# Performance work log

Hardware: AMD Instinct MI355X
Metric: run time of the kernel (lower is better)

Reference implementation:

```python
import jax, jax.numpy as jnp
import numpy as np

N = 250000   # atoms
E = 500000   # directed bond edges
B = 10000    # molecules
IN = 39      # atom feature dim (in_channels)
H = 128      # hidden_channels
ED = 10      # edge_dim
NUM_TIMESTEPS = 2


def setup_inputs() -> dict:
    key = jax.random.key(0)
    ks = iter(jax.random.split(key, 40))
    p = lambda shape: jax.random.normal(next(ks), shape, dtype=jnp.float32) * 0.05
    inp = {}
    inp["x"] = jax.random.normal(next(ks), (N, IN), dtype=jnp.float32)
    inp["edge_attr"] = jax.random.normal(next(ks), (E, ED), dtype=jnp.float32)
    # lin1
    inp["W_lin1"] = p((H, IN)); inp["b_lin1"] = p((H,))
    # GATEConv
    inp["gate_W1"] = p((H, H + ED)); inp["gate_W2"] = p((H, H))
    inp["gate_att_l"] = p((H,)); inp["gate_att_r"] = p((H,)); inp["gate_bias"] = p((H,))
    # GRUCell after GATEConv
    inp["gru1_Wih"] = p((3 * H, H)); inp["gru1_Whh"] = p((3 * H, H))
    inp["gru1_bih"] = p((3 * H,)); inp["gru1_bhh"] = p((3 * H,))
    # atom GATConv (num_layers-1 == 1)
    inp["conv_W"] = p((H, H)); inp["conv_att_src"] = p((H,)); inp["conv_att_dst"] = p((H,)); inp["conv_bias"] = p((H,))
    inp["gru2_Wih"] = p((3 * H, H)); inp["gru2_Whh"] = p((3 * H, H))
    inp["gru2_bih"] = p((3 * H,)); inp["gru2_bhh"] = p((3 * H,))
    # mol GATConv (bipartite atoms -> molecules, shared lin)
    inp["mol_W"] = p((H, H)); inp["mol_att_src"] = p((H,)); inp["mol_att_dst"] = p((H,)); inp["mol_bias"] = p((H,))
    inp["grum_Wih"] = p((3 * H, H)); inp["grum_Whh"] = p((3 * H, H))
    inp["grum_bih"] = p((3 * H,)); inp["grum_bhh"] = p((3 * H,))
    # lin2 + head
    inp["W_lin2"] = p((H, H)); inp["b_lin2"] = p((H,))
    inp["W_head"] = p((1, H)); inp["b_head"] = p((1,))
    inp["edge_index"] = jax.random.randint(next(ks), (2, E), 0, N, dtype=jnp.int32)
    inp["batch"] = jnp.sort(jax.random.randint(next(ks), (N,), 0, B, dtype=jnp.int32))
    return inp


def _gru(xg, hg, Wih, Whh, bih, bhh):
    # torch.nn.GRUCell semantics
    gi = xg @ Wih.T + bih
    gh = hg @ Whh.T + bhh
    ir, iz, inn = jnp.split(gi, 3, axis=-1)
    hr, hz, hn = jnp.split(gh, 3, axis=-1)
    r = jax.nn.sigmoid(ir + hr)
    z = jax.nn.sigmoid(iz + hz)
    n = jnp.tanh(inn + r * hn)
    return (1.0 - z) * n + z * hg


def _seg_softmax(logits, seg, num):
    # PyG softmax over target-index segments (stable, +1e-16 denom)
    m = jax.ops.segment_max(logits, seg, num_segments=num)
    e = jnp.exp(logits - m[seg])
    s = jax.ops.segment_sum(e, seg, num_segments=num)
    return e / (s[seg] + 1e-16)


def reference(x, edge_attr, W_lin1, b_lin1, gate_W1, gate_W2, gate_att_l, gate_att_r, gate_bias,
              gru1_Wih, gru1_Whh, gru1_bih, gru1_bhh,
              conv_W, conv_att_src, conv_att_dst, conv_bias,
              gru2_Wih, gru2_Whh, gru2_bih, gru2_bhh,
              mol_W, mol_att_src, mol_att_dst, mol_bias,
              grum_Wih, grum_Whh, grum_bih, grum_bhh,
              W_lin2, b_lin2, W_head, b_head,
              edge_index, batch):
    lrelu = lambda v: jax.nn.leaky_relu(v, 0.01)
    src, dst = edge_index[0], edge_index[1]  # (j, i): messages flow j -> i
    # initial atom embedding
    x = lrelu(x @ W_lin1.T + b_lin1)
    # ---- GATEConv (edge-attr-aware attention, aggr='add') ----
    xj = x[src]                                                   # [E, H]
    he = lrelu(jnp.concatenate([xj, edge_attr], axis=-1) @ gate_W1.T)
    alpha = lrelu(he @ gate_att_l + x[dst] @ gate_att_r)          # [E]
    alpha = _seg_softmax(alpha, dst, N)
    h = jax.ops.segment_sum((xj @ gate_W2.T) * alpha[:, None], dst, num_segments=N) + gate_bias
    h = jax.nn.elu(h)
    x = jax.nn.relu(_gru(h, x, gru1_Wih, gru1_Whh, gru1_bih, gru1_bhh))
    # ---- atom GATConv (heads=1, neg_slope=0.01, no self loops) ----
    xl = x @ conv_W.T
    a = lrelu((xl * conv_att_src).sum(-1)[src] + (xl * conv_att_dst).sum(-1)[dst])
    a = _seg_softmax(a, dst, N)
    h = jax.ops.segment_sum(xl[src] * a[:, None], dst, num_segments=N) + conv_bias
    h = jax.nn.relu(h)
    x = jax.nn.relu(_gru(h, x, gru2_Wih, gru2_Whh, gru2_bih, gru2_bhh))
    # ---- attentive graph readout: bipartite GAT atoms -> molecules ----
    out = jax.nn.relu(jax.ops.segment_sum(x, batch, num_segments=B))  # [B, H]
    for _ in range(NUM_TIMESTEPS):
        xs = x @ mol_W.T                                          # src transform [N, H]
        od = out @ mol_W.T                                        # dst transform [B, H]
        a = lrelu((xs * mol_att_src).sum(-1) + ((od * mol_att_dst).sum(-1))[batch])
        a = _seg_softmax(a, batch, B)
        h = jax.ops.segment_sum(xs * a[:, None], batch, num_segments=B) + mol_bias
        h = jax.nn.elu(h)
        out = jax.nn.relu(_gru(h, out, grum_Wih, grum_Whh, grum_bih, grum_bhh))
    out = out @ W_lin2.T + b_lin2
    out = out @ W_head.T + b_head                                 # [B, 1]
    return out.squeeze(-1)                                        # [B]
```

## Files before the change

### kernel.cpp

```cpp
#include <hip/hip_runtime.h>
#include <hip/hip_bf16.h>
#include <type_traits>

typedef __hip_bfloat16 bf16;

constexpr int N_  = 250000;
constexpr int E_  = 500000;
constexpr int B_  = 10000;
constexpr int H_  = 128;

typedef short s8v __attribute__((ext_vector_type(8)));
typedef float f4v __attribute__((ext_vector_type(4)));

__device__ __forceinline__ float b2f(bf16 v){ return __bfloat162float(v); }
__device__ __forceinline__ bf16  f2b(float v){ return __float2bfloat16(v); }
__device__ __forceinline__ float lrelu_f(float v){ return v > 0.f ? v : 0.01f*v; }
__device__ __forceinline__ float sigmoid_f(float x){ return __builtin_amdgcn_rcpf(1.f+__expf(-x)); }
__device__ __forceinline__ float tanh_f(float x){ return 1.f - 2.f*__builtin_amdgcn_rcpf(__expf(2.f*x)+1.f); }
__device__ __forceinline__ float elu_f(float v){ return v > 0.f ? v : __expf(v)-1.f; }
__device__ __forceinline__ unsigned f2b_bits(float f){
  bf16 h=__float2bfloat16(f); unsigned short s; __builtin_memcpy(&s,&h,2); return (unsigned)s;
}
__device__ __forceinline__ void unp8(uint4 v, float* o){
  o[0]=__uint_as_float(v.x<<16); o[1]=__uint_as_float(v.x&0xffff0000u);
  o[2]=__uint_as_float(v.y<<16); o[3]=__uint_as_float(v.y&0xffff0000u);
  o[4]=__uint_as_float(v.z<<16); o[5]=__uint_as_float(v.z&0xffff0000u);
  o[6]=__uint_as_float(v.w<<16); o[7]=__uint_as_float(v.w&0xffff0000u);
}

struct W2B { const float* s; bf16* d; int rows, ld, ow, cw; };
struct W2B9 { W2B seg[9]; };
__global__ void w2ball_k(W2B9 p){
  W2B g=p.seg[blockIdx.y];
  int i=blockIdx.x*256+threadIdx.x;
  if (i>=g.rows*g.ow) return;
  int r=i/g.ow, k=i-r*g.ow;
  g.d[i] = f2b(k<g.cw ? g.s[(size_t)r*g.ld+k] : 0.f);
}

__global__ __launch_bounds__(256) void lin1_mfma_k(const float* __restrict__ X0, const bf16* __restrict__ Wb,
                            const float* __restrict__ bias, const float* __restrict__ dvec,
                            bf16* __restrict__ Y, float* __restrict__ dout, int M){
  __shared__ __align__(16) bf16 sx[64][72];
  __shared__ float sdot[4][64];
  int wv=threadIdx.x>>6, lane=threadIdx.x&63;
  int n=lane&15, q=lane>>4;
  int c0=wv*32;
  s8v wB[2][2];
  #pragma unroll
  for (int ct=0;ct<2;ct++)
    #pragma unroll
    for (int kk=0;kk<2;kk++)
      wB[ct][kk]=*(const s8v*)(Wb+(size_t)(c0+ct*16+n)*64+kk*32+q*8);
  float bb[2];
  #pragma unroll
  for (int ct=0;ct<2;ct++) bb[ct]=bias[c0+ct*16+n];
  float va[2]={dvec[c0+n], dvec[c0+16+n]};
  for (int i=threadIdx.x;i<64*25;i+=256){ int r=i/25,k=39+(i-(i/25)*25); sx[r][k]=f2b(0.f); }
  for (long r0=(long)blockIdx.x*64; r0<M; r0+=(long)gridDim.x*64){
    __syncthreads();
    for (int f=threadIdx.x; f<64*39; f+=256){
      int r=f/39, k=f-(f/39)*39; long row=r0+r;
      sx[r][k]= f2b(row<M ? X0[row*39+k] : 0.f);
    }
    __syncthreads();
    s8v a[4][2];
    #pragma unroll
    for (int rt=0;rt<4;rt++)
      #pragma unroll
      for (int kk=0;kk<2;kk++)
        a[rt][kk]=*(const s8v*)&sx[rt*16+n][kk*32+q*8];
    f4v acc[4][2];
    #pragma unroll
    for (int rt=0;rt<4;rt++)
      #pragma unroll
      for (int ct=0;ct<2;ct++) acc[rt][ct]=(f4v){0.f,0.f,0.f,0.f};
    #pragma unroll
    for (int kk=0;kk<2;kk++)
      #pragma unroll
      for (int rt=0;rt<4;rt++)
        #pragma unroll
        for (int ct=0;ct<2;ct++)
          acc[rt][ct]=__builtin_amdgcn_mfma_f32_16x16x32_bf16(a[rt][kk],wB[ct][kk],acc[rt][ct],0,0,0);
    #pragma unroll
    for (int rt=0;rt<4;rt++){
      #pragma unroll
      for (int rg=0;rg<4;rg++){
        float y0=lrelu_f(acc[rt][0][rg]+bb[0]);
        float y1=lrelu_f(acc[rt][1][rg]+bb[1]);
        long row=r0+rt*16+q*4+rg;
        if (row<M){
          Y[row*128+c0+n]   =f2b(y0);
          Y[row*128+c0+16+n]=f2b(y1);
        }
        float pa=y0*va[0]+y1*va[1];
        #pragma unroll
        for (int o=1;o<16;o<<=1) pa+=__shfl_xor(pa,o);
        if (n==0) sdot[wv][rt*16+q*4+rg]=pa;
      }
    }
    __syncthreads();
    if (threadIdx.x<64){
      long row=r0+threadIdx.x;
      if (row<M) dout[row]=sdot[0][threadIdx.x]+sdot[1][threadIdx.x]+sdot[2][threadIdx.x]+sdot[3][threadIdx.x];
    }
  }
}

template<int ACT,int NDOT>
__global__ __launch_bounds__(256) void lin_mfma_k(const bf16* __restrict__ X, const bf16* __restrict__ Wb,
                            const float* __restrict__ bias, bf16* __restrict__ Y,
                            const float* __restrict__ v1, const float* __restrict__ v2,
                            float* __restrict__ d1, float* __restrict__ d2, int M){
  __shared__ float sdot[2][4][64];
  int wv=threadIdx.x>>6, lane=threadIdx.x&63;
  int n=lane&15, q=lane>>4;
  int c0=wv*32;
  s8v wB[2][4];
  #pragma unroll
  for (int ct=0;ct<2;ct++)
    #pragma unroll
    for (int kk=0;kk<4;kk++)
      wB[ct][kk]=*(const s8v*)(Wb+(size_t)(c0+ct*16+n)*128+kk*32+q*8);
  float bb[2];
  #pragma unroll
  for (int ct=0;ct<2;ct++) bb[ct]=bias? bias[c0+ct*16+n]:0.f;
  float va[2][2];
  if constexpr (NDOT>=1){ va[0][0]=v1[c0+n]; va[0][1]=v1[c0+16+n]; }
  if constexpr (NDOT>=2){ va[1][0]=v2[c0+n]; va[1][1]=v2[c0+16+n]; }
  for (long r0=(long)blockIdx.x*64; r0<M; r0+=(long)gridDim.x*64){
    s8v a[4][4];
    #pragma unroll
    for (int rt=0;rt<4;rt++){
      long row=r0+rt*16+n; if (row>=M) row=M-1;
      #pragma unroll
      for (int kk=0;kk<4;kk++) a[rt][kk]=*(const s8v*)(X+row*128+kk*32+q*8);
    }
    f4v acc[4][2];
    #pragma unroll
    for (int rt=0;rt<4;rt++)
      #pragma unroll
      for (int ct=0;ct<2;ct++) acc[rt][ct]=(f4v){0.f,0.f,0.f,0.f};
    #pragma unroll
    for (int kk=0;kk<4;kk++)
      #pragma unroll
      for (int rt=0;rt<4;rt++)
        #pragma unroll
        for (int ct=0;ct<2;ct++)
          acc[rt][ct]=__builtin_amdgcn_mfma_f32_16x16x32_bf16(a[rt][kk],wB[ct][kk],acc[rt][ct],0,0,0);
    #pragma unroll
    for (int rt=0;rt<4;rt++){
      #pragma unroll
      for (int rg=0;rg<4;rg++){
        float y0=acc[rt][0][rg]+bb[0];
        float y1=acc[rt][1][rg]+bb[1];
        if (ACT==2){ y0=elu_f(y0); y1=elu_f(y1); }
        long row=r0+rt*16+q*4+rg;
        if (row<M){
          Y[row*128+c0+n]   =f2b(y0);
          Y[row*128+c0+16+n]=f2b(y1);
        }
        if constexpr (NDOT>=1){
          float pa=y0*va[0][0]+y1*va[0][1];
          float pb=0.f;
          if constexpr (NDOT>=2) pb=y0*va[1][0]+y1*va[1][1];
          #pragma unroll
          for (int o=1;o<16;o<<=1){
            pa+=__shfl_xor(pa,o);
            if constexpr (NDOT>=2) pb+=__shfl_xor(pb,o);
          }
          if (n==0){
            sdot[0][wv][rt*16+q*4+rg]=pa;
            if constexpr (NDOT>=2) sdot[1][wv][rt*16+q*4+rg]=pb;
          }
        }
      }
    }
    if constexpr (NDOT>=1){
      __syncthreads();
      if (threadIdx.x<64){
        long row=r0+threadIdx.x;
        if (row<M){
          d1[row]=sdot[0][0][threadIdx.x]+sdot[0][1][threadIdx.x]+sdot[0][2][threadIdx.x]+sdot[0][3][threadIdx.x];
          if constexpr (NDOT>=2)
            d2[row]=sdot[1][0][threadIdx.x]+sdot[1][1][threadIdx.x]+sdot[1][2][threadIdx.x]+sdot[1][3][threadIdx.x];
        }
      }
      __syncthreads();
    }
  }
}

__global__ __launch_bounds__(512,1) void gru_mfma_k(const bf16* __restrict__ A, const bf16* __restrict__ X,
                            const bf16* __restrict__ Wih, const bf16* __restrict__ Whh,
                            const float* __restrict__ bih, const float* __restrict__ bhh,
                            bf16* __restrict__ dest, int M){
  __shared__ __align__(16) bf16 sA[2][32][136];
  __shared__ __align__(16) bf16 sX[2][32][136];
  int wv=threadIdx.x>>6, lane=threadIdx.x&63;
  int n=lane&15, q=lane>>4;
  int c0=wv*16;
  s8v wI[3][4], wH[3][4];
  #pragma unroll
  for (int g=0;g<3;g++)
    #pragma unroll
    for (int kk=0;kk<4;kk++){
      size_t off=((size_t)(g*128+c0+n))*128+kk*32+q*8;
      wI[g][kk]=*(const s8v*)(Wih+off);
      wH[g][kk]=*(const s8v*)(Whh+off);
    }
  int col=c0+n;
  float br =bih[col]+bhh[col];
  float bz =bih[128+col]+bhh[128+col];
  float bni=bih[256+col], bnh=bhh[256+col];

  int srow=wv*4+q;
  int schunk=n;
  long step=(long)gridDim.x*32;
  long r0=(long)blockIdx.x*32;
  int buf=0;
  {
    long rowg=r0+srow; if (rowg>=M) rowg=M-1;
    uint4 va=*(const uint4*)(A+rowg*128+schunk*8);
    uint4 vx=*(const uint4*)(X+rowg*128+schunk*8);
    *(uint4*)&sA[0][srow][schunk*8]=va;
    *(uint4*)&sX[0][srow][schunk*8]=vx;
  }
  __syncthreads();
  for (; r0<M; r0+=step){
    long rn=r0+step;
    uint4 va, vx; bool pre = rn<M;
    if (pre){
      long rowg=rn+srow; if (rowg>=M) rowg=M-1;
      va=*(const uint4*)(A+rowg*128+schunk*8);
      vx=*(const uint4*)(X+rowg*128+schunk*8);
    }
    f4v acc[6][2];
    #pragma unroll
    for (int g=0;g<6;g++)
      #pragma unroll
      for (int rt=0;rt<2;rt++) acc[g][rt]=(f4v){0.f,0.f,0.f,0.f};
    #pragma unroll
    for (int kk=0;kk<4;kk++){
      s8v aA[2], aX[2];
      #pragma unroll
      for (int rt=0;rt<2;rt++){
        aA[rt]=*(const s8v*)&sA[buf][rt*16+n][(kk*4+q)*8];
        aX[rt]=*(const s8v*)&sX[buf][rt*16+n][(kk*4+q)*8];
      }
      #pragma unroll
      for (int g=0;g<3;g++)
        #pragma unroll
        for (int rt=0;rt<2;rt++){
          acc[g  ][rt]=__builtin_amdgcn_mfma_f32_16x16x32_bf16(aA[rt],wI[g][kk],acc[g  ][rt],0,0,0);
          acc[3+g][rt]=__builtin_amdgcn_mfma_f32_16x16x32_bf16(aX[rt],wH[g][kk],acc[3+g][rt],0,0,0);
        }
    }
    float xv[2][4];
    #pragma unroll
    for (int rt=0;rt<2;rt++)
      #pragma unroll
      for (int rg=0;rg<4;rg++)
        xv[rt][rg]=b2f(sX[buf][rt*16+q*4+rg][col]);
    #pragma unroll
    for (int rt=0;rt<2;rt++){
      #pragma unroll
      for (int rg=0;rg<4;rg++){
        long row=r0+rt*16+q*4+rg;
        if (row<M){
          float rgate=sigmoid_f(acc[0][rt][rg]+acc[3][rt][rg]+br);
          float zgate=sigmoid_f(acc[1][rt][rg]+acc[4][rt][rg]+bz);
          float nn=tanh_f(acc[2][rt][rg]+bni + rgate*(acc[5][rt][rg]+bnh));
          float o=(1.f-zgate)*nn + zgate*xv[rt][rg];
          dest[row*128+col]=f2b(fmaxf(o,0.f));
        }
      }
    }
    if (pre){
      *(uint4*)&sA[buf^1][srow][schunk*8]=va;
      *(uint4*)&sX[buf^1][srow][schunk*8]=vx;
    }
    __syncthreads();
    buf^=1;
  }
}

__global__ __launch_bounds__(256) void gru_scalar_k(const float* __restrict__ A, const float* __restrict__ X,
                            const float* __restrict__ Wih, const float* __restrict__ Whh,
                            const float* __restrict__ bih, const float* __restrict__ bhh,
                            float* __restrict__ dest, int M){
  __shared__ unsigned sW[6][32*66];
  __shared__ float sA[8][132], sX[8][132];
  __shared__ float sbi[3][32], sbh[3][32];
  int c0 = blockIdx.y*32;
  for (int i=threadIdx.x; i<6*32*64; i+=256){
    int m=i>>11, r=i&2047, c=r>>6, k2=r&63;
    const float* base = (m<3)? Wih : Whh;
    int g = (m<3)? m : m-3;
    const float* wp = base + ((size_t)(g*128 + c0 + c))*128 + 2*k2;
    sW[m][c*66 + k2] = f2b_bits(wp[0]) | (f2b_bits(wp[1])<<16);
  }
  if (threadIdx.x < 96){
    int g=threadIdx.x>>5, c=threadIdx.x&31;
    sbi[g][c]=bih[g*128+c0+c]; sbh[g][c]=bhh[g*128+c0+c];
  }
  __syncthreads();
  int sub=threadIdx.x>>5, c=threadIdx.x&31;
  for (long r0=(long)blockIdx.x*8; r0<M; r0+=(long)gridDim.x*8){
    __syncthreads();
    for (int i=threadIdx.x;i<8*16;i+=256){
      int rr=i>>4, q=i&15; long row=r0+rr;
      if (row<M){
        *(float4*)&sA[rr][q*8]   = *(const float4*)(A+row*128+q*8);
        *(float4*)&sA[rr][q*8+4] = *(const float4*)(A+row*128+q*8+4);
        *(float4*)&sX[rr][q*8]   = *(const float4*)(X+row*128+q*8);
        *(float4*)&sX[rr][q*8+4] = *(const float4*)(X+row*128+q*8+4);
      } else {
        float4 z=make_float4(0,0,0,0);
        *(float4*)&sA[rr][q*8]=z; *(float4*)&sA[rr][q*8+4]=z;
        *(float4*)&sX[rr][q*8]=z; *(float4*)&sX[rr][q*8+4]=z;
      }
    }
    __syncthreads();
    long row=r0+sub;
    if (row<M){
      const unsigned* wri=&sW[0][c*66]; const unsigned* wzi=&sW[1][c*66]; const unsigned* wni=&sW[2][c*66];
      const unsigned* wrh=&sW[3][c*66]; const unsigned* wzh=&sW[4][c*66]; const unsigned* wnh=&sW[5][c*66];
      const float2* xa=(const float2*)sA[sub]; const float2* xb=(const float2*)sX[sub];
      float ari=0,azi=0,ani=0,arh=0,azh=0,anh=0;
      #pragma unroll 8
      for (int k2=0;k2<64;k2++){
        float2 av=xa[k2], bv=xb[k2];
        unsigned u;
        u=wri[k2]; ari += av.x*__uint_as_float(u<<16) + av.y*__uint_as_float(u&0xffff0000u);
        u=wzi[k2]; azi += av.x*__uint_as_float(u<<16) + av.y*__uint_as_float(u&0xffff0000u);
        u=wni[k2]; ani += av.x*__uint_as_float(u<<16) + av.y*__uint_as_float(u&0xffff0000u);
        u=wrh[k2]; arh += bv.x*__uint_as_float(u<<16) + bv.y*__uint_as_float(u&0xffff0000u);
        u=wzh[k2]; azh += bv.x*__uint_as_float(u<<16) + bv.y*__uint_as_float(u&0xffff0000u);
        u=wnh[k2]; anh += bv.x*__uint_as_float(u<<16) + bv.y*__uint_as_float(u&0xffff0000u);
      }
      float rg = sigmoid_f(ari+arh+sbi[0][c]+sbh[0][c]);
      float zg = sigmoid_f(azi+azh+sbi[1][c]+sbh[1][c]);
      float nn = tanh_f(ani+sbi[2][c] + rg*(anh+sbh[2][c]));
      float xv = sX[sub][c0+c];
      float o  = (1.f-zg)*nn + zg*xv;
      dest[row*128+c0+c] = fmaxf(o,0.f);
    }
  }
}

__global__ __launch_bounds__(256) void gate_edge_logits_k(const bf16* __restrict__ u, const float* __restrict__ ea,
                                   const float* __restrict__ gW1, const float* __restrict__ att_l,
                                   const float* __restrict__ ddst, const int* __restrict__ src,
                                   const int* __restrict__ dst, const int* __restrict__ epos,
                                   float* __restrict__ elog, int E){
  int wv=threadIdx.x>>6, lane=threadIdx.x&63;
  int t=lane&31;
  float w[10][4];
  #pragma unroll
  for (int k=0;k<10;k++)
    #pragma unroll
    for (int j=0;j<4;j++)
      w[k][j]=gW1[(size_t)(t*4+j)*138 + 128 + k];
  float al[4];
  #pragma unroll
  for (int j=0;j<4;j++) al[j]=att_l[t*4+j];

  long stride=(long)gridDim.x*8;
  long e=(long)blockIdx.x*8 + wv*2 + (lane>>5);
  if (e>=E) return;
  int sj=src[e];
  uint2 uv=*(const uint2*)(u+(size_t)sj*128+t*4);
  const float2* er=(const float2*)(ea+(size_t)e*10);
  float2 c0=er[0],c1=er[1],c2=er[2],c3=er[3],c4=er[4];
  float dv=ddst[dst[e]];
  int ep=epos[e];
  while (true){
    long en=e+stride; bool has=en<E;
    uint2 uvn=make_uint2(0,0);
    float2 d0={0,0},d1={0,0},d2={0,0},d3={0,0},d4={0,0};
    float dvn=0.f; int epn=0;
    if (has){
      int sjn=src[en];
      uvn=*(const uint2*)(u+(size_t)sjn*128+t*4);
      const float2* ern=(const float2*)(ea+(size_t)en*10);
      d0=ern[0];d1=ern[1];d2=ern[2];d3=ern[3];d4=ern[4];
      dvn=ddst[dst[en]];
      epn=epos[en];
    }
    float uf[4];
    uf[0]=__uint_as_float(uv.x<<16); uf[1]=__uint_as_float(uv.x&0xffff0000u);
    uf[2]=__uint_as_float(uv.y<<16); uf[3]=__uint_as_float(uv.y&0xffff0000u);
    float acc=0.f;
    #pragma unroll
    for (int j=0;j<4;j++){
      float v=uf[j];
      v+=c0.x*w[0][j]; v+=c0.y*w[1][j];
      v+=c1.x*w[2][j]; v+=c1.y*w[3][j];
      v+=c2.x*w[4][j]; v+=c2.y*w[5][j];
      v+=c3.x*w[6][j]; v+=c3.y*w[7][j];
      v+=c4.x*w[8][j]; v+=c4.y*w[9][j];
      acc+=lrelu_f(v)*al[j];
    }
    #pragma unroll
    for (int o=16;o;o>>=1) acc+=__shfl_xor(acc,o);
    if (t==0) elog[ep]=lrelu_f(acc+dv);
    if (!has) break;
    e=en; uv=uvn; c0=d0;c1=d1;c2=d2;c3=d3;c4=d4; dv=dvn; ep=epn;
  }
}

template<int ACT>
__global__ void node_gather_k(const float* __restrict__ elog, const int* __restrict__ srcp,
                              const int* __restrict__ ptr, const bf16* __restrict__ V,
                              const float* __restrict__ bias, bf16* __restrict__ S, int M){
  int wv=threadIdx.x>>6, lane=threadIdx.x&63;
  int g=lane>>3, t=lane&7;
  int node=blockIdx.x*32 + wv*8 + g;
  if (node>=M) return;
  int p0=ptr[node], p1=ptr[node+1];
  float m=-INFINITY;
  for (int p=p0+t;p<p1;p+=8) m=fmaxf(m,elog[p]);
  #pragma unroll
  for (int o=4;o;o>>=1) m=fmaxf(m,__shfl_xor(m,o));
  float ssum=0.f;
  float acc[16]={0,0,0,0,0,0,0,0,0,0,0,0,0,0,0,0};
  if (p0<p1){
    float lg=elog[p0];
    const uint4* vp=(const uint4*)(V+(size_t)srcp[p0]*128+t*16);
    uint4 va=vp[0], vb=vp[1];
    for (int p=p0+1;p<p1;p++){
      float lgn=elog[p];
      const uint4* vpn=(const uint4*)(V+(size_t)srcp[p]*128+t*16);
      uint4 van=vpn[0], vbn=vpn[1];
      float e=__expf(lg-m); ssum+=e;
      float xf[8]; unp8(va,xf);
      #pragma unroll
      for (int j=0;j<8;j++) acc[j]+=e*xf[j];
      unp8(vb,xf);
      #pragma unroll
      for (int j=0;j<8;j++) acc[8+j]+=e*xf[j];
      lg=lgn; va=van; vb=vbn;
    }
    float e=__expf(lg-m); ssum+=e;
    float xf[8]; unp8(va,xf);
    #pragma unroll
    for (int j=0;j<8;j++) acc[j]+=e*xf[j];
    unp8(vb,xf);
    #pragma unroll
    for (int j=0;j<8;j++) acc[8+j]+=e*xf[j];
  }
  float inv=1.f/(ssum+1e-16f);
  #pragma unroll
  for (int j=0;j<16;j++) acc[j]*=inv;
  if (ACT==1){
    #pragma unroll
    for (int j=0;j<16;j++) acc[j]=fmaxf(acc[j]+bias[t*16+j],0.f);
  }
  uint4 o1,o2;
  o1.x=f2b_bits(acc[0])|(f2b_bits(acc[1])<<16);
  o1.y=f2b_bits(acc[2])|(f2b_bits(acc[3])<<16);
  o1.z=f2b_bits(acc[4])|(f2b_bits(acc[5])<<16);
  o1.w=f2b_bits(acc[6])|(f2b_bits(acc[7])<<16);
  o2.x=f2b_bits(acc[8])|(f2b_bits(acc[9])<<16);
  o2.y=f2b_bits(acc[10])|(f2b_bits(acc[11])<<16);
  o2.z=f2b_bits(acc[12])|(f2b_bits(acc[13])<<16);
  o2.w=f2b_bits(acc[14])|(f2b_bits(acc[15])<<16);
  *(uint4*)(S+(size_t)node*128+t*16)=o1;
  *(uint4*)(S+(size_t)node*128+t*16+8)=o2;
}

__global__ __launch_bounds__(256) void conv_gather_k(const float* __restrict__ dsrc, const float* __restrict__ ddst,
    const int* __restrict__ ptr, const int* __restrict__ srcp,
    const bf16* __restrict__ V, const float* __restrict__ bias, bf16* __restrict__ S, int M){
  int wv=threadIdx.x>>6, lane=threadIdx.x&63;
  int g=lane>>3, t=lane&7;
  int node=blockIdx.x*32 + wv*8 + g;
  if (node>=M) return;
  int p0=ptr[node], p1=ptr[node+1];
  float dvn=ddst[node];
  float m=-INFINITY, s=0.f;
  float acc[16]={0,0,0,0,0,0,0,0,0,0,0,0,0,0,0,0};
  if (p0<p1){
    int sj=srcp[p0];
    float ls=dsrc[sj];
    const uint4* vp=(const uint4*)(V+(size_t)sj*128+t*16);
    uint4 va=vp[0], vb=vp[1];
    for (int p=p0+1;p<p1;p++){
      int sjn=srcp[p];
      float lsn=dsrc[sjn];
      const uint4* vpn=(const uint4*)(V+(size_t)sjn*128+t*16);
      uint4 van=vpn[0], vbn=vpn[1];
      float l=lrelu_f(ls+dvn);
      float mn=fmaxf(m,l), sc=__expf(m-mn), ee=__expf(l-mn);
      float xf[8]; unp8(va,xf);
      s=s*sc+ee;
      #pragma unroll
      for (int j=0;j<8;j++) acc[j]=acc[j]*sc+ee*xf[j];
      unp8(vb,xf);
      #pragma unroll
      for (int j=0;j<8;j++) acc[8+j]=acc[8+j]*sc+ee*xf[j];
      m=mn; ls=lsn; va=van; vb=vbn;
    }
    float l=lrelu_f(ls+dvn);
    float mn=fmaxf(m,l), sc=__expf(m-mn), ee=__expf(l-mn);
    float xf[8]; unp8(va,xf);
    s=s*sc+ee;
    #pragma unroll
    for (int j=0;j<8;j++) acc[j]=acc[j]*sc+ee*xf[j];
    unp8(vb,xf);
    #pragma unroll
    for (int j=0;j<8;j++) acc[8+j]=acc[8+j]*sc+ee*xf[j];
  }
  float inv=1.f/(s+1e-16f);
  float r[16];
  #pragma unroll
  for (int j=0;j<16;j++) r[j]=fmaxf(acc[j]*inv+bias[t*16+j],0.f);
  uint4 o1,o2;
  o1.x=f2b_bits(r[0])|(f2b_bits(r[1])<<16);
  o1.y=f2b_bits(r[2])|(f2b_bits(r[3])<<16);
  o1.z=f2b_bits(r[4])|(f2b_bits(r[5])<<16);
  o1.w=f2b_bits(r[6])|(f2b_bits(r[7])<<16);
  o2.x=f2b_bits(r[8])|(f2b_bits(r[9])<<16);
  o2.y=f2b_bits(r[10])|(f2b_bits(r[11])<<16);
  o2.z=f2b_bits(r[12])|(f2b_bits(r[13])<<16);
  o2.w=f2b_bits(r[14])|(f2b_bits(r[15])<<16);
  *(uint4*)(S+(size_t)node*128+t*16)=o1;
  *(uint4*)(S+(size_t)node*128+t*16+8)=o2;
}

__global__ void mol_ptr_k(const int* __restrict__ batch, int* __restrict__ mptr, int n, int Bn){
  int b=blockIdx.x*256+threadIdx.x; if (b>Bn) return;
  if (b==Bn){ mptr[Bn]=n; return; }
  int lo=0, hi=n;
  while (lo<hi){ int mid=(lo+hi)>>1; if (batch[mid]<b) lo=mid+1; else hi=mid; }
  mptr[b]=lo;
}

__global__ void mol_sum_k(const bf16* __restrict__ x, const int* __restrict__ mptr,
                          float* __restrict__ out, int Bn){
  int wv=threadIdx.x>>6, lane=threadIdx.x&63;
  int b=blockIdx.x*4+wv; if (b>=Bn) return;
  int p0=mptr[b], p1=mptr[b+1];
  float a0=0.f,a1=0.f;
  for (int i=p0;i<p1;i++){ a0+=b2f(x[(size_t)i*128+lane]); a1+=b2f(x[(size_t)i*128+64+lane]); }
  out[(size_t)b*128+lane]=fmaxf(a0,0.f); out[(size_t)b*128+64+lane]=fmaxf(a1,0.f);
}

__global__ void fold_att_k(const float* __restrict__ W, const float* __restrict__ att,
                           float* __restrict__ wdd){
  int k=threadIdx.x; float a=0.f;
  for (int c=0;c<128;c++) a+=att[c]*W[(size_t)c*128+k];
  wdd[k]=a;
}

__global__ __launch_bounds__(256) void mol_fused_k(const float* __restrict__ dsrc, const int* __restrict__ mptr,
    const bf16* __restrict__ xs, const float* __restrict__ wdd, const float* __restrict__ outc,
    const float* __restrict__ bias, float* __restrict__ hb, int Bn){
  int wv=threadIdx.x>>6, lane=threadIdx.x&63;
  long b=(long)blockIdx.x*4+wv; if (b>=Bn) return;
  int p0=mptr[b], p1=mptr[b+1];
  float dd=outc[(size_t)b*128+lane]*wdd[lane]+outc[(size_t)b*128+64+lane]*wdd[64+lane];
  #pragma unroll
  for (int o=32;o;o>>=1) dd+=__shfl_xor(dd,o);
  float m=-INFINITY, s=0.f, a0=0.f, a1=0.f;
  for (int i=p0;i<p1;i++){
    float a=lrelu_f(dsrc[i]+dd);
    float x0=b2f(xs[(size_t)i*128+lane]), x1=b2f(xs[(size_t)i*128+64+lane]);
    float mn=fmaxf(m,a), sc=__expf(m-mn), ee=__expf(a-mn);
    s=s*sc+ee; a0=a0*sc+ee*x0; a1=a1*sc+ee*x1; m=mn;
  }
  float inv=1.f/(s+1e-16f);
  hb[(size_t)b*128+lane]=elu_f(a0*inv+bias[lane]);
  hb[(size_t)b*128+64+lane]=elu_f(a1*inv+bias[64+lane]);
}

__global__ void fold_head_k(const float* __restrict__ W2, const float* __restrict__ b2,
                            const float* __restrict__ Wh, const float* __restrict__ bh,
                            float* __restrict__ v){
  __shared__ float sred[128];
  int k=threadIdx.x;
  float a=0.f;
  for (int c=0;c<128;c++) a+=Wh[c]*W2[(size_t)c*128+k];
  v[k]=a;
  sred[k]=b2[k]*Wh[k]; __syncthreads();
  for (int o=64;o;o>>=1){ if (k<o) sred[k]+=sred[k+o]; __syncthreads(); }
  if (k==0) v[128]=sred[0]+bh[0];
}

__global__ void head_dot_k(const float* __restrict__ out, const float* __restrict__ v,
                           float* __restrict__ y, int M){
  __shared__ float sv[129];
  if (threadIdx.x<129) sv[threadIdx.x]=v[threadIdx.x];
  __syncthreads();
  int wv=threadIdx.x>>6, lane=threadIdx.x&63;
  long row=(long)blockIdx.x*4+wv;
  if (row>=M) return;
  float a=out[row*128+lane]*sv[lane]+out[row*128+64+lane]*sv[64+lane];
  #pragma unroll
  for (int o=32;o;o>>=1) a+=__shfl_xor(a,o);
  if (!lane) y[row]=a+sv[128];
}

__global__ void zero_i32_k(int* p, int n){ int i=blockIdx.x*256+threadIdx.x; if (i<n) p[i]=0; }
__global__ void hist_k(const int* __restrict__ dst, int* __restrict__ deg, int n){
  int e=blockIdx.x*256+threadIdx.x; if (e<n) atomicAdd(&deg[dst[e]],1);
}
__global__ void scan1_k(const int* __restrict__ deg, int* __restrict__ ptr,
                        int* __restrict__ part, int n){
  __shared__ int sd[256];
  int base=blockIdx.x*1024, tid=threadIdx.x;
  int v[4]; int ssum=0;
  #pragma unroll
  for (int j=0;j<4;j++){ int idx=base+tid*4+j; v[j]= idx<n? deg[idx]:0; ssum+=v[j]; }
  sd[tid]=ssum; __syncthreads();
  for (int o=1;o<256;o<<=1){ int t = tid>=o? sd[tid-o]:0; __syncthreads(); sd[tid]+=t; __syncthreads(); }
  int excl=sd[tid]-ssum;
  #pragma unroll
  for (int j=0;j<4;j++){ int idx=base+tid*4+j; if (idx<n) ptr[idx]=excl; excl+=v[j]; }
  if (tid==255) part[blockIdx.x]=sd[255];
}
__global__ void scan2_k(int* part, int nb){
  __shared__ int sd[512];
  int tid=threadIdx.x;
  int v= tid<nb? part[tid]:0; sd[tid]=v; __syncthreads();
  for (int o=1;o<512;o<<=1){ int t = tid>=o? sd[tid-o]:0; __syncthreads(); sd[tid]+=t; __syncthreads(); }
  if (tid<nb) part[tid]=sd[tid]-v;
}
__global__ void scan3_k(int* __restrict__ ptr, const int* __restrict__ part,
                        int* __restrict__ wofs, int n, int total){
  int i=blockIdx.x*256+threadIdx.x;
  if (i<n){ int val=ptr[i]+part[i>>10]; ptr[i]=val; wofs[i]=val; }
  if (i==0) ptr[n]=total;
}
__global__ void fill_csr_k(const int* __restrict__ dst, const int* __restrict__ src,
                           int* __restrict__ wofs, int* __restrict__ srcp,
                           int* __restrict__ epos, int n){
  int e=blockIdx.x*256+threadIdx.x;
  if (e<n){ int p=atomicAdd(&wofs[dst[e]],1); srcp[p]=src[e]; epos[e]=p; }
}

extern "C" void kernel_launch(void* const* d_in, const int* in_sizes, int n_in,
                              void* d_out, int out_size, void* d_ws, size_t ws_size,
                              hipStream_t stream){
  (void)in_sizes; (void)n_in; (void)out_size; (void)ws_size;
  const float* x0        =(const float*)d_in[0];
  const float* edge_attr =(const float*)d_in[1];
  const float* W_lin1    =(const float*)d_in[2];
  const float* b_lin1    =(const float*)d_in[3];
  const float* gate_W1   =(const float*)d_in[4];
  const float* gate_W2   =(const float*)d_in[5];
  const float* gate_att_l=(const float*)d_in[6];
  const float* gate_att_r=(const float*)d_in[7];
  const float* gate_bias =(const float*)d_in[8];
  const float* g1_Wih=(const float*)d_in[9];  const float* g1_Whh=(const float*)d_in[10];
  const float* g1_bih=(const float*)d_in[11]; const float* g1_bhh=(const float*)d_in[12];
  const float* conv_W=(const float*)d_in[13];
  const float* conv_att_src=(const float*)d_in[14];
  const float* conv_att_dst=(const float*)d_in[15];
  const float* conv_bias   =(const float*)d_in[16];
  const float* g2_Wih=(const float*)d_in[17]; const float* g2_Whh=(const float*)d_in[18];
  const float* g2_bih=(const float*)d_in[19]; const float* g2_bhh=(const float*)d_in[20];
  const float* mol_W=(const float*)d_in[21];
  const float* mol_att_src=(const float*)d_in[22];
  const float* mol_att_dst=(const float*)d_in[23];
  const float* mol_bias   =(const float*)d_in[24];
  const float* gm_Wih=(const float*)d_in[25]; const float* gm_Whh=(const float*)d_in[26];
  const float* gm_bih=(const float*)d_in[27]; const float* gm_bhh=(const float*)d_in[28];
  const float* W_lin2=(const float*)d_in[29]; const float* b_lin2=(const float*)d_in[30];
  const float* W_head=(const float*)d_in[31]; const float* b_head=(const float*)d_in[32];
  const int* ei   =(const int*)d_in[33];
  const int* batch=(const int*)d_in[34];
  const int* src=ei; const int* dst=ei+E_;
  float* y=(float*)d_out;

  const size_t NH=(size_t)N_*H_, BH=(size_t)B_*H_;
  bf16* b0  =(bf16*)d_ws;
  bf16* b1  =b0+NH;
  bf16* b2v =b1+NH;
  float* outA=(float*)(b2v+NH);
  float* outB=outA+BH;
  float* hb  =outB+BH;
  float* elog=hb+BH;
  float* dsrc=elog+E_;
  float* ddst=dsrc+N_;
  float* alog=ddst+N_;
  float* wdd =alog+N_;
  float* dd  =wdd+128;
  int* deg =(int*)(dd+B_);
  int* ptr =deg+N_;
  int* wofs=ptr+N_+1;
  int* part=wofs+N_;
  int* mptr=part+512;
  int* srcp=mptr+B_+1;
  int* epos=srcp+E_;
  uintptr_t wbase=((uintptr_t)(epos+E_)+255)&~(uintptr_t)255;
  bf16* wb_gw1 =(bf16*)wbase;
  bf16* wb_gw2 =wb_gw1 +128*128;
  bf16* wb_conv=wb_gw2 +128*128;
  bf16* wb_mol =wb_conv+128*128;
  bf16* wb_g1i =wb_mol +128*128;
  bf16* wb_g1h =wb_g1i +384*128;
  bf16* wb_g2i =wb_g1h +384*128;
  bf16* wb_g2h =wb_g2i +384*128;
  bf16* wb_l1  =wb_g2h +384*128;

  W2B9 wp;
  wp.seg[0]={gate_W1,wb_gw1,128,138,128,128};
  wp.seg[1]={gate_W2,wb_gw2,128,128,128,128};
  wp.seg[2]={conv_W ,wb_conv,128,128,128,128};
  wp.seg[3]={mol_W  ,wb_mol ,128,128,128,128};
  wp.seg[4]={g1_Wih,wb_g1i,384,128,128,128};
  wp.seg[5]={g1_Whh,wb_g1h,384,128,128,128};
  wp.seg[6]={g2_Wih,wb_g2i,384,128,128,128};
  wp.seg[7]={g2_Whh,wb_g2h,384,128,128,128};
  wp.seg[8]={W_lin1,wb_l1 ,128, 39, 64, 39};
  w2ball_k<<<dim3(192,9),256,0,stream>>>(wp);

  zero_i32_k<<<(N_+255)/256,256,0,stream>>>(deg,N_);
  hist_k<<<(E_+255)/256,256,0,stream>>>(dst,deg,E_);
  int nb=(N_+1023)/1024;
  scan1_k<<<nb,256,0,stream>>>(deg,ptr,part,N_);
  scan2_k<<<1,512,0,stream>>>(part,nb);
  scan3_k<<<(N_+255)/256,256,0,stream>>>(ptr,part,wofs,N_,E_);
  fill_csr_k<<<(E_+255)/256,256,0,stream>>>(dst,src,wofs,srcp,epos,E_);
  mol_ptr_k<<<(B_+1+255)/256,256,0,stream>>>(batch,mptr,N_,B_);

  lin1_mfma_k<<<1024,256,0,stream>>>(x0,wb_l1,b_lin1,gate_att_r,b0,ddst,N_);

  const int GL=768, GN8=(N_+31)/32;
  lin_mfma_k<0,0><<<GL,256,0,stream>>>(b0,wb_gw1,nullptr,b1,nullptr,nullptr,nullptr,nullptr,N_);
  gate_edge_logits_k<<<8192,256,0,stream>>>(b1,edge_attr,gate_W1,gate_att_l,ddst,src,dst,epos,elog,E_);
  node_gather_k<0><<<GN8,256,0,stream>>>(elog,srcp,ptr,b0,nullptr,b2v,N_);
  lin_mfma_k<2,0><<<GL,256,0,stream>>>(b2v,wb_gw2,gate_bias,b1,nullptr,nullptr,nullptr,nullptr,N_);
  gru_mfma_k<<<1024,512,0,stream>>>(b1,b0,wb_g1i,wb_g1h,g1_bih,g1_bhh,b2v,N_);
  lin_mfma_k<0,2><<<GL,256,0,stream>>>(b2v,wb_conv,nullptr,b0,conv_att_src,conv_att_dst,dsrc,ddst,N_);
  conv_gather_k<<<GN8,256,0,stream>>>(dsrc,ddst,ptr,srcp,b0,conv_bias,b1,N_);
  gru_mfma_k<<<1024,512,0,stream>>>(b1,b2v,wb_g2i,wb_g2h,g2_bih,g2_bhh,b0,N_);
  mol_sum_k<<<(B_+3)/4,256,0,stream>>>(b0,mptr,outA,B_);
  lin_mfma_k<0,1><<<GL,256,0,stream>>>(b0,wb_mol,nullptr,b1,mol_att_src,nullptr,dsrc,nullptr,N_);
  fold_att_k<<<1,128,0,stream>>>(mol_W,mol_att_dst,wdd);
  float* out_cur=outA; float* out_nxt=outB;
  dim3 gm(157,4);
  for (int ts=0; ts<2; ts++){
    mol_fused_k<<<(B_+3)/4,256,0,stream>>>(dsrc,mptr,b1,wdd,out_cur,mol_bias,hb,B_);
    gru_scalar_k<<<gm,256,0,stream>>>(hb,out_cur,gm_Wih,gm_Whh,gm_bih,gm_bhh,out_nxt,B_);
    float* tmp=out_cur; out_cur=out_nxt; out_nxt=tmp;
  }
  fold_head_k<<<1,128,0,stream>>>(W_lin2,b_lin2,W_head,b_head,elog);
  head_dot_k<<<(B_+3)/4,256,0,stream>>>(out_cur,elog,y,B_);
}
```

Measured before the change: 1.068 ms.

## Reassociate GAT linear transforms after aggregation and fuse into GRU kernels

Attention logits are now computed from folded vectors (W^T att) applied to the pre-transform features, so the full N×128 projection before each gather is no longer needed. Aggregation runs on the raw features, and the 128×128 linear, bias and activation are applied afterwards inside the GRU MFMA kernel, or in a small per-molecule kernel for the readout. This removes three full-size lin_mfma passes and their writes to global memory. In exchange it adds separate row-dot kernels that read the node features again, extra LDS and MFMA work plus a sync in the GRU kernel, and different bf16 rounding points.

```diff
diff --git a/kernel.cpp b/kernel.cpp
--- a/kernel.cpp
+++ b/kernel.cpp
@@ -14,6 +14,8 @@
 
 __device__ __forceinline__ float b2f(bf16 v){ return __bfloat162float(v); }
 __device__ __forceinline__ bf16  f2b(float v){ return __float2bfloat16(v); }
+__device__ __forceinline__ float to_float(float v){ return v; }
+__device__ __forceinline__ float to_float(bf16 v){ return __bfloat162float(v); }
 __device__ __forceinline__ float lrelu_f(float v){ return v > 0.f ? v : 0.01f*v; }
 __device__ __forceinline__ float sigmoid_f(float x){ return __builtin_amdgcn_rcpf(1.f+__expf(-x)); }
 __device__ __forceinline__ float tanh_f(float x){ return 1.f - 2.f*__builtin_amdgcn_rcpf(__expf(2.f*x)+1.f); }
@@ -36,6 +38,20 @@
   if (i>=g.rows*g.ow) return;
   int r=i/g.ow, k=i-r*g.ow;
   g.d[i] = f2b(k<g.cw ? g.s[(size_t)r*g.ld+k] : 0.f);
+}
+
+__global__ void fold4_k(const float* __restrict__ Wc, const float* __restrict__ cas,
+                        const float* __restrict__ cad, const float* __restrict__ Wm,
+                        const float* __restrict__ mas, const float* __restrict__ mad,
+                        float* __restrict__ w1c, float* __restrict__ w2c,
+                        float* __restrict__ wms, float* __restrict__ wdd){
+  int k=threadIdx.x; int which=blockIdx.x;
+  const float* W  = (which<2)? Wc : Wm;
+  const float* at = (which==0)? cas : (which==1)? cad : (which==2)? mas : mad;
+  float* out = (which==0)? w1c : (which==1)? w2c : (which==2)? wms : wdd;
+  float a=0.f;
+  for (int c=0;c<128;c++) a+=at[c]*W[(size_t)c*128+k];
+  out[k]=a;
 }
 
 __global__ __launch_bounds__(256) void lin1_mfma_k(const float* __restrict__ X0, const bf16* __restrict__ Wb,
@@ -107,12 +123,9 @@
   }
 }
 
-template<int ACT,int NDOT>
+template<int ACT>
 __global__ __launch_bounds__(256) void lin_mfma_k(const bf16* __restrict__ X, const bf16* __restrict__ Wb,
-                            const float* __restrict__ bias, bf16* __restrict__ Y,
-                            const float* __restrict__ v1, const float* __restrict__ v2,
-                            float* __restrict__ d1, float* __restrict__ d2, int M){
-  __shared__ float sdot[2][4][64];
+                            const float* __restrict__ bias, bf16* __restrict__ Y, int M){
   int wv=threadIdx.x>>6, lane=threadIdx.x&63;
   int n=lane&15, q=lane>>4;
   int c0=wv*32;
@@ -125,9 +138,6 @@
   float bb[2];
   #pragma unroll
   for (int ct=0;ct<2;ct++) bb[ct]=bias? bias[c0+ct*16+n]:0.f;
-  float va[2][2];
-  if constexpr (NDOT>=1){ va[0][0]=v1[c0+n]; va[0][1]=v1[c0+16+n]; }
-  if constexpr (NDOT>=2){ va[1][0]=v2[c0+n]; va[1][1]=v2[c0+16+n]; }
   for (long r0=(long)blockIdx.x*64; r0<M; r0+=(long)gridDim.x*64){
     s8v a[4][4];
     #pragma unroll
@@ -149,58 +159,69 @@
         for (int ct=0;ct<2;ct++)
           acc[rt][ct]=__builtin_amdgcn_mfma_f32_16x16x32_bf16(a[rt][kk],wB[ct][kk],acc[rt][ct],0,0,0);
     #pragma unroll
-    for (int rt=0;rt<4;rt++){
-      #pragma unroll
-      for (int rg=0;rg<4;rg++){
-        float y0=acc[rt][0][rg]+bb[0];
-        float y1=acc[rt][1][rg]+bb[1];
-        if (ACT==2){ y0=elu_f(y0); y1=elu_f(y1); }
-        long row=r0+rt*16+q*4+rg;
-        if (row<M){
-          Y[row*128+c0+n]   =f2b(y0);
-          Y[row*128+c0+16+n]=f2b(y1);
-        }
-        if constexpr (NDOT>=1){
-          float pa=y0*va[0][0]+y1*va[0][1];
-          float pb=0.f;
-          if constexpr (NDOT>=2) pb=y0*va[1][0]+y1*va[1][1];
-          #pragma unroll
-          for (int o=1;o<16;o<<=1){
-            pa+=__shfl_xor(pa,o);
-            if constexpr (NDOT>=2) pb+=__shfl_xor(pb,o);
-          }
-          if (n==0){
-            sdot[0][wv][rt*16+q*4+rg]=pa;
-            if constexpr (NDOT>=2) sdot[1][wv][rt*16+q*4+rg]=pb;
+    for (int ct=0;ct<2;ct++){
+      int col=c0+ct*16+n;
+      #pragma unroll
+      for (int rt=0;rt<4;rt++){
+        #pragma unroll
+        for (int rg=0;rg<4;rg++){
+          long row=r0+rt*16+q*4+rg;
+          if (row<M){
+            float v=acc[rt][ct][rg]+bb[ct];
+            if (ACT==2) v=elu_f(v);
+            Y[row*128+col]=f2b(v);
           }
         }
       }
     }
-    if constexpr (NDOT>=1){
-      __syncthreads();
-      if (threadIdx.x<64){
-        long row=r0+threadIdx.x;
-        if (row<M){
-          d1[row]=sdot[0][0][threadIdx.x]+sdot[0][1][threadIdx.x]+sdot[0][2][threadIdx.x]+sdot[0][3][threadIdx.x];
-          if constexpr (NDOT>=2)
-            d2[row]=sdot[1][0][threadIdx.x]+sdot[1][1][threadIdx.x]+sdot[1][2][threadIdx.x]+sdot[1][3][threadIdx.x];
-        }
-      }
-      __syncthreads();
-    }
-  }
-}
-
-__global__ __launch_bounds__(512,1) void gru_mfma_k(const bf16* __restrict__ A, const bf16* __restrict__ X,
+  }
+}
+
+template<typename TY>
+__global__ void rowdot_k(const TY* __restrict__ Y, const float* __restrict__ v,
+                         float* __restrict__ d, int M){
+  __shared__ float sv[128];
+  if (threadIdx.x<128) sv[threadIdx.x]=v[threadIdx.x];
+  __syncthreads();
+  int wv=threadIdx.x>>6, lane=threadIdx.x&63;
+  long row=(long)blockIdx.x*4+wv;
+  if (row>=M) return;
+  float a=to_float(Y[row*128+lane])*sv[lane]+to_float(Y[row*128+64+lane])*sv[64+lane];
+  #pragma unroll
+  for (int o=32;o;o>>=1) a+=__shfl_xor(a,o);
+  if (!lane) d[row]=a;
+}
+
+__global__ void rowdot2_k(const bf16* __restrict__ Y, const float* __restrict__ v1,
+                          const float* __restrict__ v2, float* __restrict__ d1,
+                          float* __restrict__ d2, int M){
+  __shared__ float sv1[128], sv2[128];
+  if (threadIdx.x<128){ sv1[threadIdx.x]=v1[threadIdx.x]; sv2[threadIdx.x]=v2[threadIdx.x]; }
+  __syncthreads();
+  int wv=threadIdx.x>>6, lane=threadIdx.x&63;
+  long row=(long)blockIdx.x*4+wv;
+  if (row>=M) return;
+  float x0=b2f(Y[row*128+lane]), x1=b2f(Y[row*128+64+lane]);
+  float a=x0*sv1[lane]+x1*sv1[64+lane];
+  float b=x0*sv2[lane]+x1*sv2[64+lane];
+  #pragma unroll
+  for (int o=32;o;o>>=1){ a+=__shfl_xor(a,o); b+=__shfl_xor(b,o); }
+  if (!lane){ d1[row]=a; d2[row]=b; }
+}
+
+template<int ACT>
+__global__ __launch_bounds__(512,1) void gru_gw2_mfma_k(const bf16* __restrict__ S, const bf16* __restrict__ X,
+                            const bf16* __restrict__ Wg, const float* __restrict__ gbias,
                             const bf16* __restrict__ Wih, const bf16* __restrict__ Whh,
                             const float* __restrict__ bih, const float* __restrict__ bhh,
                             bf16* __restrict__ dest, int M){
-  __shared__ __align__(16) bf16 sA[2][32][136];
+  __shared__ __align__(16) bf16 sS[2][32][136];
   __shared__ __align__(16) bf16 sX[2][32][136];
+  __shared__ __align__(16) bf16 sA[32][136];
   int wv=threadIdx.x>>6, lane=threadIdx.x&63;
   int n=lane&15, q=lane>>4;
   int c0=wv*16;
-  s8v wI[3][4], wH[3][4];
+  s8v wI[3][4], wH[3][4], wG[4];
   #pragma unroll
   for (int g=0;g<3;g++)
     #pragma unroll
@@ -209,7 +230,11 @@
       wI[g][kk]=*(const s8v*)(Wih+off);
       wH[g][kk]=*(const s8v*)(Whh+off);
     }
+  #pragma unroll
+  for (int kk=0;kk<4;kk++)
+    wG[kk]=*(const s8v*)(Wg+(size_t)(c0+n)*128+kk*32+q*8);
   int col=c0+n;
+  float bA =gbias[col];
   float br =bih[col]+bhh[col];
   float bz =bih[128+col]+bhh[128+col];
   float bni=bih[256+col], bnh=bhh[256+col];
@@ -221,20 +246,39 @@
   int buf=0;
   {
     long rowg=r0+srow; if (rowg>=M) rowg=M-1;
-    uint4 va=*(const uint4*)(A+rowg*128+schunk*8);
+    uint4 vs=*(const uint4*)(S+rowg*128+schunk*8);
     uint4 vx=*(const uint4*)(X+rowg*128+schunk*8);
-    *(uint4*)&sA[0][srow][schunk*8]=va;
+    *(uint4*)&sS[0][srow][schunk*8]=vs;
     *(uint4*)&sX[0][srow][schunk*8]=vx;
   }
   __syncthreads();
   for (; r0<M; r0+=step){
     long rn=r0+step;
-    uint4 va, vx; bool pre = rn<M;
+    uint4 vs, vx; bool pre = rn<M;
     if (pre){
       long rowg=rn+srow; if (rowg>=M) rowg=M-1;
-      va=*(const uint4*)(A+rowg*128+schunk*8);
+      vs=*(const uint4*)(S+rowg*128+schunk*8);
       vx=*(const uint4*)(X+rowg*128+schunk*8);
     }
+    f4v accA[2];
+    accA[0]=(f4v){0.f,0.f,0.f,0.f}; accA[1]=(f4v){0.f,0.f,0.f,0.f};
+    #pragma unroll
+    for (int kk=0;kk<4;kk++){
+      #pragma unroll
+      for (int rt=0;rt<2;rt++){
+        s8v aS=*(const s8v*)&sS[buf][rt*16+n][(kk*4+q)*8];
+        accA[rt]=__builtin_amdgcn_mfma_f32_16x16x32_bf16(aS,wG[kk],accA[rt],0,0,0);
+      }
+    }
+    #pragma unroll
+    for (int rt=0;rt<2;rt++)
+      #pragma unroll
+      for (int rg=0;rg<4;rg++){
+        float av=accA[rt][rg]+bA;
+        av = (ACT==1)? fmaxf(av,0.f) : elu_f(av);
+        sA[rt*16+q*4+rg][col]=f2b(av);
+      }
+    __syncthreads();
     f4v acc[6][2];
     #pragma unroll
     for (int g=0;g<6;g++)
@@ -245,7 +289,7 @@
       s8v aA[2], aX[2];
       #pragma unroll
       for (int rt=0;rt<2;rt++){
-        aA[rt]=*(const s8v*)&sA[buf][rt*16+n][(kk*4+q)*8];
+        aA[rt]=*(const s8v*)&sA[rt*16+n][(kk*4+q)*8];
         aX[rt]=*(const s8v*)&sX[buf][rt*16+n][(kk*4+q)*8];
       }
       #pragma unroll
@@ -277,7 +321,7 @@
       }
     }
     if (pre){
-      *(uint4*)&sA[buf^1][srow][schunk*8]=va;
+      *(uint4*)&sS[buf^1][srow][schunk*8]=vs;
       *(uint4*)&sX[buf^1][srow][schunk*8]=vx;
     }
     __syncthreads();
@@ -453,10 +497,6 @@
   float inv=1.f/(ssum+1e-16f);
   #pragma unroll
   for (int j=0;j<16;j++) acc[j]*=inv;
-  if (ACT==1){
-    #pragma unroll
-    for (int j=0;j<16;j++) acc[j]=fmaxf(acc[j]+bias[t*16+j],0.f);
-  }
   uint4 o1,o2;
   o1.x=f2b_bits(acc[0])|(f2b_bits(acc[1])<<16);
   o1.y=f2b_bits(acc[2])|(f2b_bits(acc[3])<<16);
@@ -470,9 +510,9 @@
   *(uint4*)(S+(size_t)node*128+t*16+8)=o2;
 }
 
-__global__ __launch_bounds__(256) void conv_gather_k(const float* __restrict__ dsrc, const float* __restrict__ ddst,
+__global__ __launch_bounds__(256) void conv_gather_raw_k(const float* __restrict__ dsrc, const float* __restrict__ ddst,
     const int* __restrict__ ptr, const int* __restrict__ srcp,
-    const bf16* __restrict__ V, const float* __restrict__ bias, bf16* __restrict__ S, int M){
+    const bf16* __restrict__ V, bf16* __restrict__ S, int M){
   int wv=threadIdx.x>>6, lane=threadIdx.x&63;
   int g=lane>>3, t=lane&7;
   int node=blockIdx.x*32 + wv*8 + g;
@@ -513,18 +553,17 @@
     for (int j=0;j<8;j++) acc[8+j]=acc[8+j]*sc+ee*xf[j];
   }
   float inv=1.f/(s+1e-16f);
-  float r[16];
-  #pragma unroll
-  for (int j=0;j<16;j++) r[j]=fmaxf(acc[j]*inv+bias[t*16+j],0.f);
+  #pragma unroll
+  for (int j=0;j<16;j++) acc[j]*=inv;
   uint4 o1,o2;
-  o1.x=f2b_bits(r[0])|(f2b_bits(r[1])<<16);
-  o1.y=f2b_bits(r[2])|(f2b_bits(r[3])<<16);
-  o1.z=f2b_bits(r[4])|(f2b_bits(r[5])<<16);
-  o1.w=f2b_bits(r[6])|(f2b_bits(r[7])<<16);
-  o2.x=f2b_bits(r[8])|(f2b_bits(r[9])<<16);
-  o2.y=f2b_bits(r[10])|(f2b_bits(r[11])<<16);
-  o2.z=f2b_bits(r[12])|(f2b_bits(r[13])<<16);
-  o2.w=f2b_bits(r[14])|(f2b_bits(r[15])<<16);
+  o1.x=f2b_bits(acc[0])|(f2b_bits(acc[1])<<16);
+  o1.y=f2b_bits(acc[2])|(f2b_bits(acc[3])<<16);
+  o1.z=f2b_bits(acc[4])|(f2b_bits(acc[5])<<16);
+  o1.w=f2b_bits(acc[6])|(f2b_bits(acc[7])<<16);
+  o2.x=f2b_bits(acc[8])|(f2b_bits(acc[9])<<16);
+  o2.y=f2b_bits(acc[10])|(f2b_bits(acc[11])<<16);
+  o2.z=f2b_bits(acc[12])|(f2b_bits(acc[13])<<16);
+  o2.w=f2b_bits(acc[14])|(f2b_bits(acc[15])<<16);
   *(uint4*)(S+(size_t)node*128+t*16)=o1;
   *(uint4*)(S+(size_t)node*128+t*16+8)=o2;
 }
@@ -547,16 +586,9 @@
   out[(size_t)b*128+lane]=fmaxf(a0,0.f); out[(size_t)b*128+64+lane]=fmaxf(a1,0.f);
 }
 
-__global__ void fold_att_k(const float* __restrict__ W, const float* __restrict__ att,
-                           float* __restrict__ wdd){
-  int k=threadIdx.x; float a=0.f;
-  for (int c=0;c<128;c++) a+=att[c]*W[(size_t)c*128+k];
-  wdd[k]=a;
-}
-
-__global__ __launch_bounds__(256) void mol_fused_k(const float* __restrict__ dsrc, const int* __restrict__ mptr,
-    const bf16* __restrict__ xs, const float* __restrict__ wdd, const float* __restrict__ outc,
-    const float* __restrict__ bias, float* __restrict__ hb, int Bn){
+__global__ __launch_bounds__(256) void mol_fused_raw_k(const float* __restrict__ dsrc, const int* __restrict__ mptr,
+    const bf16* __restrict__ x, const float* __restrict__ wdd, const float* __restrict__ outc,
+    float* __restrict__ P, int Bn){
   int wv=threadIdx.x>>6, lane=threadIdx.x&63;
   long b=(long)blockIdx.x*4+wv; if (b>=Bn) return;
   int p0=mptr[b], p1=mptr[b+1];
@@ -566,13 +598,44 @@
   float m=-INFINITY, s=0.f, a0=0.f, a1=0.f;
   for (int i=p0;i<p1;i++){
     float a=lrelu_f(dsrc[i]+dd);
-    float x0=b2f(xs[(size_t)i*128+lane]), x1=b2f(xs[(size_t)i*128+64+lane]);
+    float x0=b2f(x[(size_t)i*128+lane]), x1=b2f(x[(size_t)i*128+64+lane]);
     float mn=fmaxf(m,a), sc=__expf(m-mn), ee=__expf(a-mn);
     s=s*sc+ee; a0=a0*sc+ee*x0; a1=a1*sc+ee*x1; m=mn;
   }
   float inv=1.f/(s+1e-16f);
-  hb[(size_t)b*128+lane]=elu_f(a0*inv+bias[lane]);
-  hb[(size_t)b*128+64+lane]=elu_f(a1*inv+bias[64+lane]);
+  P[(size_t)b*128+lane]=a0*inv;
+  P[(size_t)b*128+64+lane]=a1*inv;
+}
+
+__global__ __launch_bounds__(256) void mol_lin_k(const float* __restrict__ P, const float* __restrict__ W,
+                         const float* __restrict__ bias, float* __restrict__ hb, int Bn){
+  __shared__ bf16 sW[128][132];
+  __shared__ float sP[8][128];
+  __shared__ float sb[128];
+  for (int i=threadIdx.x;i<128*128;i+=256){ int r=i>>7,k=i&127; sW[r][k]=f2b(W[i]); }
+  if (threadIdx.x<128) sb[threadIdx.x]=bias[threadIdx.x];
+  __syncthreads();
+  int sub=threadIdx.x>>5, c0=threadIdx.x&31;
+  for (long b0=(long)blockIdx.x*8; b0<Bn; b0+=(long)gridDim.x*8){
+    __syncthreads();
+    for (int i=threadIdx.x;i<8*32;i+=256){
+      int rr=i>>5,q=i&31; long b=b0+rr;
+      *(float4*)&sP[rr][q*4] = (b<Bn)? *(const float4*)(P+b*128+q*4) : make_float4(0,0,0,0);
+    }
+    __syncthreads();
+    long b=b0+sub;
+    if (b<Bn){
+      float acc[4]={0,0,0,0};
+      #pragma unroll 4
+      for (int k=0;k<128;k++){
+        float pv=sP[sub][k];
+        #pragma unroll
+        for (int j=0;j<4;j++) acc[j]+=pv*b2f(sW[c0+32*j][k]);
+      }
+      #pragma unroll
+      for (int j=0;j<4;j++) hb[b*128+c0+32*j]=elu_f(acc[j]+sb[c0+32*j]);
+    }
+  }
 }
 
 __global__ void fold_head_k(const float* __restrict__ W2, const float* __restrict__ b2,
@@ -704,6 +767,9 @@
   bf16* wb_g2i =wb_g1h +384*128;
   bf16* wb_g2h =wb_g2i +384*128;
   bf16* wb_l1  =wb_g2h +384*128;
+  float* w1c = dd;
+  float* w2c = dd+128;
+  float* wms = dd+256;
 
   W2B9 wp;
   wp.seg[0]={gate_W1,wb_gw1,128,138,128,128};
@@ -716,6 +782,8 @@
   wp.seg[7]={g2_Whh,wb_g2h,384,128,128,128};
   wp.seg[8]={W_lin1,wb_l1 ,128, 39, 64, 39};
   w2ball_k<<<dim3(192,9),256,0,stream>>>(wp);
+  fold4_k<<<4,128,0,stream>>>(conv_W,conv_att_src,conv_att_dst,mol_W,mol_att_src,mol_att_dst,
+                              w1c,w2c,wms,wdd);
 
   zero_i32_k<<<(N_+255)/256,256,0,stream>>>(deg,N_);
   hist_k<<<(E_+255)/256,256,0,stream>>>(dst,deg,E_);
@@ -728,22 +796,22 @@
 
   lin1_mfma_k<<<1024,256,0,stream>>>(x0,wb_l1,b_lin1,gate_att_r,b0,ddst,N_);
 
-  const int GL=768, GN8=(N_+31)/32;
-  lin_mfma_k<0,0><<<GL,256,0,stream>>>(b0,wb_gw1,nullptr,b1,nullptr,nullptr,nullptr,nullptr,N_);
+  const int GL=768, GN8=(N_+31)/32, GN4=(N_+3)/4;
+  lin_mfma_k<0><<<GL,256,0,stream>>>(b0,wb_gw1,nullptr,b1,N_);
   gate_edge_logits_k<<<8192,256,0,stream>>>(b1,edge_attr,gate_W1,gate_att_l,ddst,src,dst,epos,elog,E_);
   node_gather_k<0><<<GN8,256,0,stream>>>(elog,srcp,ptr,b0,nullptr,b2v,N_);
-  lin_mfma_k<2,0><<<GL,256,0,stream>>>(b2v,wb_gw2,gate_bias,b1,nullptr,nullptr,nullptr,nullptr,N_);
-  gru_mfma_k<<<1024,512,0,stream>>>(b1,b0,wb_g1i,wb_g1h,g1_bih,g1_bhh,b2v,N_);
-  lin_mfma_k<0,2><<<GL,256,0,stream>>>(b2v,wb_conv,nullptr,b0,conv_att_src,conv_att_dst,dsrc,ddst,N_);
-  conv_gather_k<<<GN8,256,0,stream>>>(dsrc,ddst,ptr,srcp,b0,conv_bias,b1,N_);
-  gru_mfma_k<<<1024,512,0,stream>>>(b1,b2v,wb_g2i,wb_g2h,g2_bih,g2_bhh,b0,N_);
+  gru_gw2_mfma_k<2><<<1024,512,0,stream>>>(b2v,b0,wb_gw2,gate_bias,wb_g1i,wb_g1h,g1_bih,g1_bhh,b2v,N_);
+  rowdot2_k<<<GN4,256,0,stream>>>(b2v,w1c,w2c,dsrc,ddst,N_);
+  conv_gather_raw_k<<<GN8,256,0,stream>>>(dsrc,ddst,ptr,srcp,b2v,b1,N_);
+  gru_gw2_mfma_k<1><<<1024,512,0,stream>>>(b1,b2v,wb_conv,conv_bias,wb_g2i,wb_g2h,g2_bih,g2_bhh,b0,N_);
   mol_sum_k<<<(B_+3)/4,256,0,stream>>>(b0,mptr,outA,B_);
-  lin_mfma_k<0,1><<<GL,256,0,stream>>>(b0,wb_mol,nullptr,b1,mol_att_src,nullptr,dsrc,nullptr,N_);
-  fold_att_k<<<1,128,0,stream>>>(mol_W,mol_att_dst,wdd);
+  rowdot_k<bf16><<<GN4,256,0,stream>>>(b0,wms,dsrc,N_);
   float* out_cur=outA; float* out_nxt=outB;
   dim3 gm(157,4);
   for (int ts=0; ts<2; ts++){
-    mol_fused_k<<<(B_+3)/4,256,0,stream>>>(dsrc,mptr,b1,wdd,out_cur,mol_bias,hb,B_);
+    float* P=out_nxt;
+    mol_fused_raw_k<<<(B_+3)/4,256,0,stream>>>(dsrc,mptr,b0,wdd,out_cur,P,B_);
+    mol_lin_k<<<256,256,0,stream>>>(P,mol_W,mol_bias,hb,B_);
     gru_scalar_k<<<gm,256,0,stream>>>(hb,out_cur,gm_Wih,gm_Whh,gm_bih,gm_bhh,out_nxt,B_);
     float* tmp=out_cur; out_cur=out_nxt; out_nxt=tmp;
   }
```

Result: slower. 1.096 ms (+2.7%).
